# Kernel optimization log

Hardware: AMD Instinct MI355X
Metric: run time of the kernel (lower is better)

## Reference

```python
import jax, jax.numpy as jnp
import numpy as np

N_NODES = 50000
N_EDGES = 1600000
DIM = 128
SLOPE = 0.2  # LeakyReLU negative slope


def setup_inputs() -> dict:
    key = jax.random.key(0)
    ks = jax.random.split(key, 9)
    indices = jax.random.randint(ks[0], (2, N_EDGES), 0, N_NODES)
    features = jax.random.normal(ks[1], (N_NODES, DIM), dtype=jnp.float32)
    W1_w = jax.random.normal(ks[2], (DIM, DIM), dtype=jnp.float32) * 0.05
    W1_b = jax.random.normal(ks[3], (DIM,), dtype=jnp.float32) * 0.05
    W2_w = jax.random.normal(ks[4], (DIM, DIM), dtype=jnp.float32) * 0.05
    W2_b = jax.random.normal(ks[5], (DIM,), dtype=jnp.float32) * 0.05
    Watt_w = jax.random.normal(ks[6], (DIM, DIM), dtype=jnp.float32) * 0.05
    Watt_b = jax.random.normal(ks[7], (DIM,), dtype=jnp.float32) * 0.05
    a = jax.random.normal(ks[8], (2 * DIM, 1), dtype=jnp.float32) * 0.05
    return {"indices": indices, "features": features, "num_nodes": N_NODES,
            "W1_w": W1_w, "W1_b": W1_b, "W2_w": W2_w, "W2_b": W2_b,
            "Watt_w": Watt_w, "Watt_b": Watt_b, "a": a}


def reference(indices, features, num_nodes, W1_w, W1_b, W2_w, W2_b, Watt_w, Watt_b, a):
    src, dst = indices[0], indices[1]
    d = W1_w.shape[1]
    # attention scores: e_ij = leakyrelu(cat(h_src, h_dst) @ a) == h_src@a1 + h_dst@a2
    h_att = features @ Watt_w + Watt_b                      # [N, d]
    a1, a2 = a[:d], a[d:]                                    # each [d, 1]
    e = jax.nn.leaky_relu(h_att[src] @ a1 + h_att[dst] @ a2, SLOPE)  # [E, 1]
    # global-max-stabilized segment softmax over incoming edges of dst
    e = e - jnp.max(e)
    exp_e = jnp.exp(e)                                       # [E, 1]
    denom = jax.ops.segment_sum(exp_e, dst, num_segments=num_nodes)  # [N, 1]
    alpha = exp_e / (denom[dst] + 1e-9)                      # [E, 1]
    # weighted message aggregation
    h_msg = features @ W1_w + W1_b                           # [N, d]
    weighted = h_msg[src] * alpha                            # [E, d]
    h_neigh = jax.ops.segment_sum(weighted, dst, num_segments=num_nodes)  # [N, d]
    # in_dim == out_dim -> h_self = features (module skips extra W1)
    h_self = features
    sum_h = h_self + h_neigh
    prod_h = h_self * h_neigh
    return jax.nn.leaky_relu(sum_h + prod_h @ W2_w + W2_b, SLOPE)
```

## Files before the change

### kernel.cpp

```cpp
#include <hip/hip_runtime.h>

#define DIM 128
#define SLOPE 0.2f
#define NPBK 64
#define SLAB 4000
#define CHUNK_A 8192
#define EPT 32
#define KMAX 1024
#define WT_STRIDE 136

typedef __attribute__((ext_vector_type(8))) short bf16x8;
typedef __attribute__((ext_vector_type(4))) float f32x4;

__device__ __forceinline__ float leaky(float x) { return x > 0.f ? x : SLOPE * x; }

__device__ __forceinline__ unsigned short f2bf(float x) {
    unsigned u = __float_as_uint(x);
    return (unsigned short)((u + 0x7FFFu + ((u >> 16) & 1u)) >> 16);
}
__device__ __forceinline__ float bf2f(unsigned short h) {
    return __uint_as_float(((unsigned)h) << 16);
}
__device__ __forceinline__ bf16x8 pack_bf16x8(float4 a, float4 b) {
    bf16x8 r;
    r[0] = (short)f2bf(a.x); r[1] = (short)f2bf(a.y);
    r[2] = (short)f2bf(a.z); r[3] = (short)f2bf(a.w);
    r[4] = (short)f2bf(b.x); r[5] = (short)f2bf(b.y);
    r[6] = (short)f2bf(b.z); r[7] = (short)f2bf(b.w);
    return r;
}

__global__ void k_prep(const float* __restrict__ Watt_w, const float* __restrict__ Watt_b,
                       const float* __restrict__ a, float* __restrict__ v1,
                       float* __restrict__ v2, float* __restrict__ c12) {
    int k = threadIdx.x;
    __shared__ float a1s[DIM], a2s[DIM];
    __shared__ float r1[DIM], r2[DIM];
    a1s[k] = a[k];
    a2s[k] = a[DIM + k];
    __syncthreads();
    float acc1 = 0.f, acc2 = 0.f;
    const float* row = Watt_w + (size_t)k * DIM;
    for (int j = 0; j < DIM; ++j) {
        float w = row[j];
        acc1 += w * a1s[j];
        acc2 += w * a2s[j];
    }
    v1[k] = acc1;
    v2[k] = acc2;
    float b = Watt_b[k];
    r1[k] = b * a1s[k];
    r2[k] = b * a2s[k];
    __syncthreads();
    for (int off = 64; off > 0; off >>= 1) {
        if (k < off) { r1[k] += r1[k + off]; r2[k] += r2[k + off]; }
        __syncthreads();
    }
    if (k == 0) { c12[0] = r1[0]; c12[1] = r2[0]; }
}

__global__ __launch_bounds__(256) void k_fused_fwd(
    const float* __restrict__ feat, const float* __restrict__ W1,
    const float* __restrict__ W1b, const float* __restrict__ v1,
    const float* __restrict__ v2, const float* __restrict__ c12,
    unsigned short* __restrict__ h_msg, float* __restrict__ s1, float* __restrict__ s2,
    const int* __restrict__ src, const int* __restrict__ dst,
    int* __restrict__ bucket_cur, int* __restrict__ ebuf,
    int n_nodes, int n_tiles16, int n_edges, int K, int nb_part, int total_waves) {
    __shared__ union {
        struct { unsigned short Wt[DIM * WT_STRIDE]; float v1s[DIM]; float v2s[DIM]; } g;
        struct { int h[KMAX]; int lcur[KMAX]; } p;
    } sm;
    int tid = threadIdx.x;

    if (blockIdx.x < nb_part) {
        int* h = sm.p.h;
        int* lcur = sm.p.lcur;
        for (int i = tid; i < KMAX; i += 256) h[i] = 0;
        __syncthreads();
        int cbase = blockIdx.x * CHUNK_A;
        int pval[EPT], pb[EPT];
        #pragma unroll
        for (int p = 0; p < 8; ++p) {
            int i0 = cbase + p * 1024 + tid * 4;
            if (i0 + 3 < n_edges) {
                int4 d = *(const int4*)&dst[i0];
                int4 s = *(const int4*)&src[i0];
                int b0 = d.x >> 6, b1 = d.y >> 6, b2 = d.z >> 6, b3 = d.w >> 6;
                atomicAdd(&h[b0], 1); atomicAdd(&h[b1], 1);
                atomicAdd(&h[b2], 1); atomicAdd(&h[b3], 1);
                pb[p * 4 + 0] = b0; pval[p * 4 + 0] = ((d.x & 63) << 17) | s.x;
                pb[p * 4 + 1] = b1; pval[p * 4 + 1] = ((d.y & 63) << 17) | s.y;
                pb[p * 4 + 2] = b2; pval[p * 4 + 2] = ((d.z & 63) << 17) | s.z;
                pb[p * 4 + 3] = b3; pval[p * 4 + 3] = ((d.w & 63) << 17) | s.w;
            } else {
                #pragma unroll
                for (int k = 0; k < 4; ++k) {
                    int i = i0 + k;
                    if (i < n_edges) {
                        int d = dst[i], s = src[i];
                        int b = d >> 6;
                        atomicAdd(&h[b], 1);
                        pb[p * 4 + k] = b;
                        pval[p * 4 + k] = ((d & 63) << 17) | s;
                    } else {
                        pb[p * 4 + k] = -1;
                        pval[p * 4 + k] = 0;
                    }
                }
            }
        }
        __syncthreads();
        for (int i = tid; i < K; i += 256) {
            int c = h[i];
            lcur[i] = c ? (i * SLAB + atomicAdd(&bucket_cur[i], c)) : 0;
        }
        __syncthreads();
        #pragma unroll
        for (int k = 0; k < EPT; ++k) {
            int b = pb[k];
            if (b >= 0) {
                int pos = atomicAdd(&lcur[b], 1);
                ebuf[pos] = pval[k];
            }
        }
        return;
    }

    unsigned short* Wt = sm.g.Wt;
    float* v1s = sm.g.v1s;
    float* v2s = sm.g.v2s;
    for (int i = tid; i < DIM * DIM; i += 256) {
        int k = i >> 7, n = i & 127;
        Wt[n * WT_STRIDE + k] = f2bf(W1[i]);
    }
    if (tid < DIM) { v1s[tid] = v1[tid]; v2s[tid] = v2[tid]; }
    __syncthreads();

    int lane = tid & 63, wid = tid >> 6;
    int ln15 = lane & 15, q = lane >> 4;
    float c1 = c12[0], c2 = c12[1];
    float bias[8];
    #pragma unroll
    for (int nt = 0; nt < 8; ++nt) bias[nt] = W1b[nt * 16 + ln15];

    for (int t = (blockIdx.x - nb_part) * 4 + wid; t < n_tiles16; t += total_waves) {
        int base = t * 16;
        int row = base + ln15;
        bool valid = row < n_nodes;
        const float* frow = feat + (size_t)row * DIM;
        bf16x8 afr[4];
        float p1 = 0.f, p2 = 0.f;
        #pragma unroll
        for (int kc = 0; kc < 4; ++kc) {
            int col0 = kc * 32 + q * 8;
            float4 u0 = {0.f, 0.f, 0.f, 0.f}, u1 = {0.f, 0.f, 0.f, 0.f};
            if (valid) {
                u0 = *(const float4*)&frow[col0];
                u1 = *(const float4*)&frow[col0 + 4];
            }
            float4 wa = *(const float4*)&v1s[col0];
            float4 wb = *(const float4*)&v1s[col0 + 4];
            float4 wc = *(const float4*)&v2s[col0];
            float4 wd = *(const float4*)&v2s[col0 + 4];
            p1 += u0.x * wa.x + u0.y * wa.y + u0.z * wa.z + u0.w * wa.w
                + u1.x * wb.x + u1.y * wb.y + u1.z * wb.z + u1.w * wb.w;
            p2 += u0.x * wc.x + u0.y * wc.y + u0.z * wc.z + u0.w * wc.w
                + u1.x * wd.x + u1.y * wd.y + u1.z * wd.z + u1.w * wd.w;
            afr[kc] = pack_bf16x8(u0, u1);
        }
        p1 += __shfl_xor(p1, 16, 64); p1 += __shfl_xor(p1, 32, 64);
        p2 += __shfl_xor(p2, 16, 64); p2 += __shfl_xor(p2, 32, 64);
        if (q == 0 && valid) { s1[row] = p1 + c1; s2[row] = p2 + c2; }

        f32x4 acc[8];
        #pragma unroll
        for (int nt = 0; nt < 8; ++nt)
            acc[nt] = (f32x4){bias[nt], bias[nt], bias[nt], bias[nt]};
        #pragma unroll
        for (int kc = 0; kc < 4; ++kc) {
            #pragma unroll
            for (int nt = 0; nt < 8; ++nt) {
                bf16x8 b = *(const bf16x8*)&Wt[(nt * 16 + ln15) * WT_STRIDE + kc * 32 + q * 8];
                acc[nt] = __builtin_amdgcn_mfma_f32_16x16x32_bf16(afr[kc], b, acc[nt], 0, 0, 0);
            }
        }
        #pragma unroll
        for (int nt = 0; nt < 8; ++nt) {
            #pragma unroll
            for (int r = 0; r < 4; ++r) {
                int rr = base + q * 4 + r;
                if (rr < n_nodes)
                    h_msg[(size_t)rr * DIM + nt * 16 + ln15] = f2bf(acc[nt][r]);
            }
        }
    }
}

__global__ __launch_bounds__(1024, 8) void k_back(
    const int* __restrict__ ebuf, const int* __restrict__ bucket_cur,
    const float* __restrict__ s1, const float* __restrict__ s2,
    const unsigned short* __restrict__ h_msg, const float* __restrict__ feat,
    const float* __restrict__ W2, const float* __restrict__ W2b,
    float* __restrict__ out, int n_nodes, int K) {
    __shared__ unsigned short Wt[DIM * WT_STRIDE];
    __shared__ unsigned short sorted_s[SLAB];
    __shared__ unsigned short tile_hn[NPBK * DIM];
    __shared__ int bins[NPBK], scn_[NPBK], cur[NPBK];
    __shared__ int next_node;

    int tid = threadIdx.x;
    int b = blockIdx.x;
    int base_node = b * NPBK;
    int start = b * SLAB;
    int cnt = bucket_cur[b];

    for (int i = tid; i < DIM * DIM; i += 1024) {
        int k = i >> 7, n = i & 127;
        Wt[n * WT_STRIDE + k] = f2bf(W2[i]);
    }
    if (tid < NPBK) bins[tid] = 0;
    if (tid == 0) next_node = 0;
    __syncthreads();

    for (int i = tid; i < cnt; i += 1024)
        atomicAdd(&bins[((unsigned)ebuf[start + i]) >> 17], 1);
    __syncthreads();
    if (tid < NPBK) scn_[tid] = bins[tid];
    __syncthreads();
    for (int off = 1; off < NPBK; off <<= 1) {
        int v = (tid < NPBK && tid >= off) ? scn_[tid - off] : 0;
        __syncthreads();
        if (tid < NPBK) scn_[tid] += v;
        __syncthreads();
    }
    if (tid < NPBK) cur[tid] = scn_[tid] - bins[tid];
    __syncthreads();
    for (int i = tid; i < cnt; i += 1024) {
        int v = ebuf[start + i];
        int p = atomicAdd(&cur[v >> 17], 1);
        sorted_s[p] = (unsigned short)(v & 0xFFFF);
    }
    __syncthreads();

    int lane = tid & 31;
    while (true) {
        int g_local;
        if (lane == 0) g_local = atomicAdd(&next_node, 1);
        g_local = __shfl(g_local, 0, 32);
        if (g_local >= NPBK) break;
        int g = base_node + g_local;
        if (g >= n_nodes) {
            *(ushort4*)&tile_hn[g_local * DIM + lane * 4] = (ushort4){0, 0, 0, 0};
            continue;
        }
        int begin = scn_[g_local] - bins[g_local];
        int end = scn_[g_local];
        float s2d = s2[g];
        float4 accA = {0.f, 0.f, 0.f, 0.f}, accB = {0.f, 0.f, 0.f, 0.f};
        float wA = 0.f, wB = 0.f;
        int j = begin;
        int iA = (j < end) ? (int)sorted_s[j] : 0;
        int iB = (j + 1 < end) ? (int)sorted_s[j + 1] : 0;
        float pA = s1[iA], pB = s1[iB];
        while (j + 1 < end) {
            int cA = iA, cB = iB;
            float sA = pA, sB = pB;
            int jn = j + 2;
            if (jn < end)     iA = (int)sorted_s[jn];
            if (jn + 1 < end) iB = (int)sorted_s[jn + 1];
            pA = s1[iA]; pB = s1[iB];
            ushort4 uA = *(const ushort4*)&h_msg[(size_t)cA * DIM + lane * 4];
            ushort4 uB = *(const ushort4*)&h_msg[(size_t)cB * DIM + lane * 4];
            float eA = __expf(leaky(sA + s2d));
            float eB = __expf(leaky(sB + s2d));
            accA.x += eA * bf2f(uA.x); accA.y += eA * bf2f(uA.y);
            accA.z += eA * bf2f(uA.z); accA.w += eA * bf2f(uA.w);
            wA += eA;
            accB.x += eB * bf2f(uB.x); accB.y += eB * bf2f(uB.y);
            accB.z += eB * bf2f(uB.z); accB.w += eB * bf2f(uB.w);
            wB += eB;
            j = jn;
        }
        if (j < end) {
            int cA = iA;
            ushort4 uA = *(const ushort4*)&h_msg[(size_t)cA * DIM + lane * 4];
            float eA = __expf(leaky(pA + s2d));
            accA.x += eA * bf2f(uA.x); accA.y += eA * bf2f(uA.y);
            accA.z += eA * bf2f(uA.z); accA.w += eA * bf2f(uA.w);
            wA += eA;
        }
        float inv = 1.f / (wA + wB + 1e-9f);
        ushort4 o;
        o.x = f2bf((accA.x + accB.x) * inv);
        o.y = f2bf((accA.y + accB.y) * inv);
        o.z = f2bf((accA.z + accB.z) * inv);
        o.w = f2bf((accA.w + accB.w) * inv);
        *(ushort4*)&tile_hn[g_local * DIM + lane * 4] = o;
    }
    __syncthreads();

    int w = tid >> 6;
    int lane64 = tid & 63;
    int ln15 = lane64 & 15, q = lane64 >> 4;
    int tile = w >> 2;
    int nt0 = (w & 3) * 2;
    int lrow = tile * 16 + ln15;
    int grow = base_node + lrow;
    bool valid = grow < n_nodes;
    const float* frow = feat + (size_t)grow * DIM;
    bf16x8 afr[4];
    #pragma unroll
    for (int kc = 0; kc < 4; ++kc) {
        int col0 = kc * 32 + q * 8;
        float4 p0 = {0.f, 0.f, 0.f, 0.f}, p1 = {0.f, 0.f, 0.f, 0.f};
        bf16x8 hn8 = *(const bf16x8*)&tile_hn[lrow * DIM + col0];
        if (valid) {
            float4 f0 = *(const float4*)&frow[col0];
            float4 f1 = *(const float4*)&frow[col0 + 4];
            p0.x = f0.x * bf2f((unsigned short)hn8[0]);
            p0.y = f0.y * bf2f((unsigned short)hn8[1]);
            p0.z = f0.z * bf2f((unsigned short)hn8[2]);
            p0.w = f0.w * bf2f((unsigned short)hn8[3]);
            p1.x = f1.x * bf2f((unsigned short)hn8[4]);
            p1.y = f1.y * bf2f((unsigned short)hn8[5]);
            p1.z = f1.z * bf2f((unsigned short)hn8[6]);
            p1.w = f1.w * bf2f((unsigned short)hn8[7]);
        }
        afr[kc] = pack_bf16x8(p0, p1);
    }
    f32x4 acc0, acc1;
    {
        float b0 = W2b[(nt0 + 0) * 16 + ln15];
        float b1 = W2b[(nt0 + 1) * 16 + ln15];
        acc0 = (f32x4){b0, b0, b0, b0};
        acc1 = (f32x4){b1, b1, b1, b1};
    }
    #pragma unroll
    for (int kc = 0; kc < 4; ++kc) {
        bf16x8 w0 = *(const bf16x8*)&Wt[((nt0 + 0) * 16 + ln15) * WT_STRIDE + kc * 32 + q * 8];
        bf16x8 w1 = *(const bf16x8*)&Wt[((nt0 + 1) * 16 + ln15) * WT_STRIDE + kc * 32 + q * 8];
        acc0 = __builtin_amdgcn_mfma_f32_16x16x32_bf16(afr[kc], w0, acc0, 0, 0, 0);
        acc1 = __builtin_amdgcn_mfma_f32_16x16x32_bf16(afr[kc], w1, acc1, 0, 0, 0);
    }
    #pragma unroll
    for (int r = 0; r < 4; ++r) {
        int rl = tile * 16 + q * 4 + r;
        int rr = base_node + rl;
        if (rr < n_nodes) {
            int colA = (nt0 + 0) * 16 + ln15;
            int colB = (nt0 + 1) * 16 + ln15;
            float fA = feat[(size_t)rr * DIM + colA];
            float fB = feat[(size_t)rr * DIM + colB];
            float hA = bf2f(tile_hn[rl * DIM + colA]);
            float hB = bf2f(tile_hn[rl * DIM + colB]);
            out[(size_t)rr * DIM + colA] = leaky(fA + hA + acc0[r]);
            out[(size_t)rr * DIM + colB] = leaky(fB + hB + acc1[r]);
        }
    }
}

extern "C" void kernel_launch(void* const* d_in, const int* in_sizes, int n_in,
                              void* d_out, int out_size, void* d_ws, size_t ws_size,
                              hipStream_t stream) {
    const int*   indices = (const int*)d_in[0];
    const float* feat    = (const float*)d_in[1];
    const float* W1w  = (const float*)d_in[3];
    const float* W1b  = (const float*)d_in[4];
    const float* W2w  = (const float*)d_in[5];
    const float* W2b  = (const float*)d_in[6];
    const float* Wattw = (const float*)d_in[7];
    const float* Wattb = (const float*)d_in[8];
    const float* a     = (const float*)d_in[9];

    int n_edges = in_sizes[0] / 2;
    int n_nodes = in_sizes[1] / DIM;
    int n_tiles16 = (n_nodes + 15) / 16;
    int K = (n_nodes + NPBK - 1) / NPBK;
    const int* src = indices;
    const int* dst = indices + n_edges;

    float* ws      = (float*)d_ws;
    unsigned short* h_msg = (unsigned short*)ws;
    int*   ebuf    = (int*)(h_msg + (size_t)n_nodes * DIM);
    float* s1      = (float*)(ebuf + (size_t)K * SLAB);
    float* s2      = s1 + n_nodes;
    float* v1      = s2 + n_nodes;
    float* v2      = v1 + DIM;
    float* c12     = v2 + DIM;
    int*   bucket_cur = (int*)(c12 + 2);

    hipMemsetAsync(bucket_cur, 0, (size_t)KMAX * sizeof(int), stream);

    k_prep<<<1, 128, 0, stream>>>(Wattw, Wattb, a, v1, v2, c12);
    {
        int nb_part = (n_edges + CHUNK_A - 1) / CHUNK_A;
        int gemm_blocks = 512;
        k_fused_fwd<<<nb_part + gemm_blocks, 256, 0, stream>>>(
            feat, W1w, W1b, v1, v2, c12, h_msg, s1, s2,
            src, dst, bucket_cur, ebuf,
            n_nodes, n_tiles16, n_edges, K, nb_part, gemm_blocks * 4);
    }
    k_back<<<K, 1024, 0, stream>>>(ebuf, bucket_cur, s1, s2, h_msg, feat,
                                   W2w, W2b, (float*)d_out, n_nodes, K);
}
```

Baseline: 216.1 us.

## Split back kernel into quarter-bucket blocks and precompute edge weights

The aggregation kernel now launches four 256-thread blocks per 64-node bucket instead of one 1024-thread block. Each block filters the bucket's edges down to its own 16 destination nodes and stores a packed source index plus a bf16 exp weight per edge, so s1 gathers and exp leave the inner loop. The W2 bf16 transpose moves into the prep kernel and is read from global memory rather than rebuilt in LDS by every block. The trade-off is that each block rescans the whole bucket's edge list twice, the weights lose precision by being stored in bf16, and QCAP=1024 is assumed large enough for the edges of 16 nodes.

```diff
diff --git a/kernel.cpp b/kernel.cpp
--- a/kernel.cpp
+++ b/kernel.cpp
@@ -4,10 +4,12 @@
 #define SLOPE 0.2f
 #define NPBK 64
 #define SLAB 4000
+#define QCAP 1024
 #define CHUNK_A 8192
 #define EPT 32
 #define KMAX 1024
 #define WT_STRIDE 136
+#define TSTRIDE 136
 
 typedef __attribute__((ext_vector_type(8))) short bf16x8;
 typedef __attribute__((ext_vector_type(4))) float f32x4;
@@ -31,8 +33,9 @@
 }
 
 __global__ void k_prep(const float* __restrict__ Watt_w, const float* __restrict__ Watt_b,
-                       const float* __restrict__ a, float* __restrict__ v1,
-                       float* __restrict__ v2, float* __restrict__ c12) {
+                       const float* __restrict__ a, const float* __restrict__ W2,
+                       float* __restrict__ v1, float* __restrict__ v2,
+                       float* __restrict__ c12, unsigned short* __restrict__ Wt_g) {
     int k = threadIdx.x;
     __shared__ float a1s[DIM], a2s[DIM];
     __shared__ float r1[DIM], r2[DIM];
@@ -57,6 +60,10 @@
         __syncthreads();
     }
     if (k == 0) { c12[0] = r1[0]; c12[1] = r2[0]; }
+    for (int i = k; i < DIM * DIM; i += 128) {
+        int kk = i >> 7, n = i & 127;
+        Wt_g[n * DIM + kk] = f2bf(W2[i]);
+    }
 }
 
 __global__ __launch_bounds__(256) void k_fused_fwd(
@@ -197,83 +204,83 @@
     }
 }
 
-__global__ __launch_bounds__(1024, 8) void k_back(
+__global__ __launch_bounds__(256, 6) void k_back(
     const int* __restrict__ ebuf, const int* __restrict__ bucket_cur,
     const float* __restrict__ s1, const float* __restrict__ s2,
     const unsigned short* __restrict__ h_msg, const float* __restrict__ feat,
-    const float* __restrict__ W2, const float* __restrict__ W2b,
-    float* __restrict__ out, int n_nodes, int K) {
-    __shared__ unsigned short Wt[DIM * WT_STRIDE];
-    __shared__ unsigned short sorted_s[SLAB];
-    __shared__ unsigned short tile_hn[NPBK * DIM];
-    __shared__ int bins[NPBK], scn_[NPBK], cur[NPBK];
+    const unsigned short* __restrict__ Wt_g, const float* __restrict__ W2b,
+    float* __restrict__ out, int n_nodes) {
+    __shared__ int psorted[QCAP];
+    __shared__ unsigned short tile_hn[16 * TSTRIDE];
+    __shared__ float s2loc[16];
+    __shared__ int bins16[16], scn16[16], cur16[16];
     __shared__ int next_node;
 
     int tid = threadIdx.x;
-    int b = blockIdx.x;
-    int base_node = b * NPBK;
+    int b = blockIdx.x >> 2;
+    int qid = blockIdx.x & 3;
+    int base16 = b * NPBK + qid * 16;
     int start = b * SLAB;
     int cnt = bucket_cur[b];
 
-    for (int i = tid; i < DIM * DIM; i += 1024) {
-        int k = i >> 7, n = i & 127;
-        Wt[n * WT_STRIDE + k] = f2bf(W2[i]);
-    }
-    if (tid < NPBK) bins[tid] = 0;
+    if (tid < 16) {
+        bins16[tid] = 0;
+        int g = base16 + tid;
+        s2loc[tid] = (g < n_nodes) ? s2[g] : 0.f;
+    }
     if (tid == 0) next_node = 0;
     __syncthreads();
 
-    for (int i = tid; i < cnt; i += 1024)
-        atomicAdd(&bins[((unsigned)ebuf[start + i]) >> 17], 1);
-    __syncthreads();
-    if (tid < NPBK) scn_[tid] = bins[tid];
-    __syncthreads();
-    for (int off = 1; off < NPBK; off <<= 1) {
-        int v = (tid < NPBK && tid >= off) ? scn_[tid - off] : 0;
-        __syncthreads();
-        if (tid < NPBK) scn_[tid] += v;
-        __syncthreads();
-    }
-    if (tid < NPBK) cur[tid] = scn_[tid] - bins[tid];
-    __syncthreads();
-    for (int i = tid; i < cnt; i += 1024) {
+    for (int i = tid; i < cnt; i += 256) {
         int v = ebuf[start + i];
-        int p = atomicAdd(&cur[v >> 17], 1);
-        sorted_s[p] = (unsigned short)(v & 0xFFFF);
+        int dl = v >> 17;
+        if ((dl >> 4) == qid) atomicAdd(&bins16[dl & 15], 1);
+    }
+    __syncthreads();
+    if (tid == 0) {
+        int run = 0;
+        for (int k = 0; k < 16; ++k) { scn16[k] = run; cur16[k] = run; run += bins16[k]; }
+    }
+    __syncthreads();
+    for (int i = tid; i < cnt; i += 256) {
+        int v = ebuf[start + i];
+        int dl = v >> 17;
+        if ((dl >> 4) == qid) {
+            int s = v & 0x1FFFF;
+            int p = atomicAdd(&cur16[dl & 15], 1);
+            float e = __expf(leaky(s1[s] + s2loc[dl & 15]));
+            psorted[p] = s | (((int)f2bf(e)) << 16);
+        }
     }
     __syncthreads();
 
     int lane = tid & 31;
     while (true) {
-        int g_local;
-        if (lane == 0) g_local = atomicAdd(&next_node, 1);
-        g_local = __shfl(g_local, 0, 32);
-        if (g_local >= NPBK) break;
-        int g = base_node + g_local;
+        int gl;
+        if (lane == 0) gl = atomicAdd(&next_node, 1);
+        gl = __shfl(gl, 0, 32);
+        if (gl >= 16) break;
+        int g = base16 + gl;
         if (g >= n_nodes) {
-            *(ushort4*)&tile_hn[g_local * DIM + lane * 4] = (ushort4){0, 0, 0, 0};
+            *(ushort4*)&tile_hn[gl * TSTRIDE + lane * 4] = (ushort4){0, 0, 0, 0};
             continue;
         }
-        int begin = scn_[g_local] - bins[g_local];
-        int end = scn_[g_local];
-        float s2d = s2[g];
+        int begin = scn16[gl];
+        int end = begin + bins16[gl];
         float4 accA = {0.f, 0.f, 0.f, 0.f}, accB = {0.f, 0.f, 0.f, 0.f};
         float wA = 0.f, wB = 0.f;
         int j = begin;
-        int iA = (j < end) ? (int)sorted_s[j] : 0;
-        int iB = (j + 1 < end) ? (int)sorted_s[j + 1] : 0;
-        float pA = s1[iA], pB = s1[iB];
+        int vA = (j < end) ? psorted[j] : 0;
+        int vB = (j + 1 < end) ? psorted[j + 1] : 0;
         while (j + 1 < end) {
-            int cA = iA, cB = iB;
-            float sA = pA, sB = pB;
+            int cA = vA & 0xFFFF, cB = vB & 0xFFFF;
+            float eA = bf2f((unsigned short)(((unsigned)vA) >> 16));
+            float eB = bf2f((unsigned short)(((unsigned)vB) >> 16));
             int jn = j + 2;
-            if (jn < end)     iA = (int)sorted_s[jn];
-            if (jn + 1 < end) iB = (int)sorted_s[jn + 1];
-            pA = s1[iA]; pB = s1[iB];
+            if (jn < end)     vA = psorted[jn];
+            if (jn + 1 < end) vB = psorted[jn + 1];
             ushort4 uA = *(const ushort4*)&h_msg[(size_t)cA * DIM + lane * 4];
             ushort4 uB = *(const ushort4*)&h_msg[(size_t)cB * DIM + lane * 4];
-            float eA = __expf(leaky(sA + s2d));
-            float eB = __expf(leaky(sB + s2d));
             accA.x += eA * bf2f(uA.x); accA.y += eA * bf2f(uA.y);
             accA.z += eA * bf2f(uA.z); accA.w += eA * bf2f(uA.w);
             wA += eA;
@@ -283,9 +290,9 @@
             j = jn;
         }
         if (j < end) {
-            int cA = iA;
+            int cA = vA & 0xFFFF;
+            float eA = bf2f((unsigned short)(((unsigned)vA) >> 16));
             ushort4 uA = *(const ushort4*)&h_msg[(size_t)cA * DIM + lane * 4];
-            float eA = __expf(leaky(pA + s2d));
             accA.x += eA * bf2f(uA.x); accA.y += eA * bf2f(uA.y);
             accA.z += eA * bf2f(uA.z); accA.w += eA * bf2f(uA.w);
             wA += eA;
@@ -296,17 +303,15 @@
         o.y = f2bf((accA.y + accB.y) * inv);
         o.z = f2bf((accA.z + accB.z) * inv);
         o.w = f2bf((accA.w + accB.w) * inv);
-        *(ushort4*)&tile_hn[g_local * DIM + lane * 4] = o;
+        *(ushort4*)&tile_hn[gl * TSTRIDE + lane * 4] = o;
     }
     __syncthreads();
 
     int w = tid >> 6;
     int lane64 = tid & 63;
     int ln15 = lane64 & 15, q = lane64 >> 4;
-    int tile = w >> 2;
-    int nt0 = (w & 3) * 2;
-    int lrow = tile * 16 + ln15;
-    int grow = base_node + lrow;
+    int nt0 = w * 2;
+    int grow = base16 + ln15;
     bool valid = grow < n_nodes;
     const float* frow = feat + (size_t)grow * DIM;
     bf16x8 afr[4];
@@ -314,7 +319,7 @@
     for (int kc = 0; kc < 4; ++kc) {
         int col0 = kc * 32 + q * 8;
         float4 p0 = {0.f, 0.f, 0.f, 0.f}, p1 = {0.f, 0.f, 0.f, 0.f};
-        bf16x8 hn8 = *(const bf16x8*)&tile_hn[lrow * DIM + col0];
+        bf16x8 hn8 = *(const bf16x8*)&tile_hn[ln15 * TSTRIDE + col0];
         if (valid) {
             float4 f0 = *(const float4*)&frow[col0];
             float4 f1 = *(const float4*)&frow[col0 + 4];
@@ -338,22 +343,22 @@
     }
     #pragma unroll
     for (int kc = 0; kc < 4; ++kc) {
-        bf16x8 w0 = *(const bf16x8*)&Wt[((nt0 + 0) * 16 + ln15) * WT_STRIDE + kc * 32 + q * 8];
-        bf16x8 w1 = *(const bf16x8*)&Wt[((nt0 + 1) * 16 + ln15) * WT_STRIDE + kc * 32 + q * 8];
+        bf16x8 w0 = *(const bf16x8*)&Wt_g[((nt0 + 0) * 16 + ln15) * DIM + kc * 32 + q * 8];
+        bf16x8 w1 = *(const bf16x8*)&Wt_g[((nt0 + 1) * 16 + ln15) * DIM + kc * 32 + q * 8];
         acc0 = __builtin_amdgcn_mfma_f32_16x16x32_bf16(afr[kc], w0, acc0, 0, 0, 0);
         acc1 = __builtin_amdgcn_mfma_f32_16x16x32_bf16(afr[kc], w1, acc1, 0, 0, 0);
     }
     #pragma unroll
     for (int r = 0; r < 4; ++r) {
-        int rl = tile * 16 + q * 4 + r;
-        int rr = base_node + rl;
+        int rl = q * 4 + r;
+        int rr = base16 + rl;
         if (rr < n_nodes) {
             int colA = (nt0 + 0) * 16 + ln15;
             int colB = (nt0 + 1) * 16 + ln15;
             float fA = feat[(size_t)rr * DIM + colA];
             float fB = feat[(size_t)rr * DIM + colB];
-            float hA = bf2f(tile_hn[rl * DIM + colA]);
-            float hB = bf2f(tile_hn[rl * DIM + colB]);
+            float hA = bf2f(tile_hn[rl * TSTRIDE + colA]);
+            float hB = bf2f(tile_hn[rl * TSTRIDE + colB]);
             out[(size_t)rr * DIM + colA] = leaky(fA + hA + acc0[r]);
             out[(size_t)rr * DIM + colB] = leaky(fB + hB + acc1[r]);
         }
@@ -389,10 +394,11 @@
     float* v2      = v1 + DIM;
     float* c12     = v2 + DIM;
     int*   bucket_cur = (int*)(c12 + 2);
+    unsigned short* Wt_g = (unsigned short*)(bucket_cur + KMAX);
 
     hipMemsetAsync(bucket_cur, 0, (size_t)KMAX * sizeof(int), stream);
 
-    k_prep<<<1, 128, 0, stream>>>(Wattw, Wattb, a, v1, v2, c12);
+    k_prep<<<1, 128, 0, stream>>>(Wattw, Wattb, a, W2w, v1, v2, c12, Wt_g);
     {
         int nb_part = (n_edges + CHUNK_A - 1) / CHUNK_A;
         int gemm_blocks = 512;
@@ -401,6 +407,6 @@
             src, dst, bucket_cur, ebuf,
             n_nodes, n_tiles16, n_edges, K, nb_part, gemm_blocks * 4);
     }
-    k_back<<<K, 1024, 0, stream>>>(ebuf, bucket_cur, s1, s2, h_msg, feat,
-                                   W2w, W2b, (float*)d_out, n_nodes, K);
-}
+    k_back<<<K * 4, 256, 0, stream>>>(ebuf, bucket_cur, s1, s2, h_msg, feat,
+                                      Wt_g, W2b, (float*)d_out, n_nodes);
+}
```

After: 239.9 us. +11.0%, slower.
